# Performance work log

Hardware: AMD Instinct MI355X
Metric: run time of the kernel (lower is better)

Reference implementation:

```python
import jax, jax.numpy as jnp
import numpy as np


def relu_bt(x):
    # -threshold(-leaky_relu(x), -t, -t) == min(leaky_relu(x), t), t = ||x||_inf (detached)
    t = jax.lax.stop_gradient(jnp.max(jnp.abs(x)))
    return jnp.minimum(jax.nn.leaky_relu(x, negative_slope=0.01), t)


def setup_inputs() -> dict:
    key = jax.random.key(0)
    k1, k2, k3, k4 = jax.random.split(key, 4)
    N, E, F_in, F_out = 100000, 1600000, 128, 64
    x = jax.random.normal(k1, (N, F_in), dtype=jnp.float32)
    edge_index = jax.random.randint(k2, (2, E), 0, N, dtype=jnp.int64)
    # xavier_normal with gain=1.414
    W = jax.random.normal(k3, (F_in, F_out), dtype=jnp.float32) * (1.414 * np.sqrt(2.0 / (F_in + F_out)))
    a = jax.random.normal(k4, (1, 4 * F_out), dtype=jnp.float32) * (1.414 * np.sqrt(2.0 / (1 + 4 * F_out)))
    return {"x": x, "edge_index": edge_index, "W": W, "a": a}


def reference(x, edge_index, W, a):
    N = x.shape[0]
    F_out = W.shape[1]
    h = x @ W  # [N, F_out]
    src = edge_index[0]
    dst = edge_index[1]
    hs = h[src]  # [E, F_out]
    hd = h[dst]  # [E, F_out]
    agg = relu_bt(hs + hd)
    diff = relu_bt(hs - hd)
    # a @ cat([hs, hd, agg, diff], dim=1).T == sum of four per-edge dot products
    a0, a1, a2, a3 = jnp.split(a.reshape(4 * F_out), 4)
    score = hs @ a0 + hd @ a1 + agg @ a2 + diff @ a3  # [E]
    edge_e = jnp.exp(-relu_bt(score))  # [E]
    # spmm(A, ones): rowsum over outgoing edges (grouped by src)
    e_rowsum = jax.ops.segment_sum(edge_e, src, num_segments=N)  # [N]
    # spmm(A, h): weighted aggregation of neighbor (dst) features into src rows
    h_prime = jax.ops.segment_sum(edge_e[:, None] * hd, src, num_segments=N)  # [N, F_out]
    return h_prime / (e_rowsum[:, None] + 1e-16)
```

## Files before the change

### kernel.cpp

```cpp
#include <hip/hip_runtime.h>
#include <hip/hip_fp16.h>

#define F_IN 128
#define F_OUT 64
#define BIN_TILE 2048
#define BSHIFT 6
#define BNODES 64
#define BCAP 2048u

#define LK_A 0.505f
#define LK_B 0.495f

__device__ __forceinline__ float leaky(float v) {
    return fmaf(LK_B, fabsf(v), LK_A * v);
}

template <int CTRL>
__device__ __forceinline__ float dppadd(float v) {
    return v + __builtin_bit_cast(float,
        __builtin_amdgcn_update_dpp(0, __builtin_bit_cast(int, v), CTRL, 0xf, 0xf, true));
}

__device__ __forceinline__ float sum8(float v) {
    v = dppadd<0xB1>(v);
    v = dppadd<0x4E>(v);
    v = dppadd<0x141>(v);
    return v;
}

__device__ __forceinline__ float xslot_sum2(float v) {
    v = dppadd<0x128>(v);
    v += __shfl_xor(v, 16);
    return v;
}

__device__ __forceinline__ float wave_sum(float v) {
    v += __builtin_bit_cast(float, __builtin_amdgcn_update_dpp(0, __builtin_bit_cast(int, v), 0x111, 0xf, 0xf, true));
    v += __builtin_bit_cast(float, __builtin_amdgcn_update_dpp(0, __builtin_bit_cast(int, v), 0x112, 0xf, 0xf, true));
    v += __builtin_bit_cast(float, __builtin_amdgcn_update_dpp(0, __builtin_bit_cast(int, v), 0x114, 0xf, 0xe, true));
    v += __builtin_bit_cast(float, __builtin_amdgcn_update_dpp(0, __builtin_bit_cast(int, v), 0x118, 0xf, 0xc, true));
    v += __builtin_bit_cast(float, __builtin_amdgcn_update_dpp(0, __builtin_bit_cast(int, v), 0x142, 0xa, 0xf, true));
    v += __builtin_bit_cast(float, __builtin_amdgcn_update_dpp(0, __builtin_bit_cast(int, v), 0x143, 0xc, 0xf, true));
    return __builtin_bit_cast(float, __builtin_amdgcn_readlane(__builtin_bit_cast(int, v), 63));
}

__device__ __forceinline__ void cvt8(const uint4 u, float* g) {
    float2 f;
    f = __half22float2(__builtin_bit_cast(__half2, u.x)); g[0] = f.x; g[1] = f.y;
    f = __half22float2(__builtin_bit_cast(__half2, u.y)); g[2] = f.x; g[3] = f.y;
    f = __half22float2(__builtin_bit_cast(__half2, u.z)); g[4] = f.x; g[5] = f.y;
    f = __half22float2(__builtin_bit_cast(__half2, u.w)); g[6] = f.x; g[7] = f.y;
}

__global__ __launch_bounds__(256) void gemm_binA(const float* __restrict__ x,
                                                 const float* __restrict__ W,
                                                 float* __restrict__ h32,
                                                 uint2* __restrict__ h16,
                                                 const int* __restrict__ ei,
                                                 unsigned* __restrict__ gcur,
                                                 unsigned* __restrict__ binned,
                                                 int N, int E, int NB, int ngemm,
                                                 unsigned cap, int mode) {
    __shared__ unsigned smem_u[8192];

    if ((int)blockIdx.x < ngemm) {
        float (*w_lds)[F_OUT] = (float (*)[F_OUT])smem_u;
        {
            const float4* Wv = (const float4*)W;
            float4* wl = (float4*)w_lds;
            for (int i = threadIdx.x; i < F_IN * F_OUT / 4; i += 256) wl[i] = Wv[i];
        }
        __syncthreads();

        const int cg = threadIdx.x & 15;
        const int rs = threadIdx.x >> 4;
        const int row0 = blockIdx.x * 128 + rs * 8;

        int r[8];
#pragma unroll
        for (int i = 0; i < 8; ++i) { const int rr = row0 + i; r[i] = rr < N ? rr : N - 1; }

        float4 acc[8];
#pragma unroll
        for (int i = 0; i < 8; ++i) acc[i] = make_float4(0.f, 0.f, 0.f, 0.f);

        float4 xc[8];
#pragma unroll
        for (int i = 0; i < 8; ++i) xc[i] = *(const float4*)(x + (size_t)r[i] * F_IN);

        for (int k4 = 0; k4 < 32; ++k4) {
            float4 xn[8];
            if (k4 < 31) {
#pragma unroll
                for (int i = 0; i < 8; ++i)
                    xn[i] = *(const float4*)(x + (size_t)r[i] * F_IN + (k4 + 1) * 4);
            }
            float4 wv[4];
#pragma unroll
            for (int kk = 0; kk < 4; ++kk)
                wv[kk] = *(const float4*)&w_lds[k4 * 4 + kk][cg * 4];

#pragma unroll
            for (int i = 0; i < 8; ++i) {
                acc[i].x = fmaf(xc[i].x, wv[0].x, acc[i].x);
                acc[i].y = fmaf(xc[i].x, wv[0].y, acc[i].y);
                acc[i].z = fmaf(xc[i].x, wv[0].z, acc[i].z);
                acc[i].w = fmaf(xc[i].x, wv[0].w, acc[i].w);
                acc[i].x = fmaf(xc[i].y, wv[1].x, acc[i].x);
                acc[i].y = fmaf(xc[i].y, wv[1].y, acc[i].y);
                acc[i].z = fmaf(xc[i].y, wv[1].z, acc[i].z);
                acc[i].w = fmaf(xc[i].y, wv[1].w, acc[i].w);
                acc[i].x = fmaf(xc[i].z, wv[2].x, acc[i].x);
                acc[i].y = fmaf(xc[i].z, wv[2].y, acc[i].y);
                acc[i].z = fmaf(xc[i].z, wv[2].z, acc[i].z);
                acc[i].w = fmaf(xc[i].z, wv[2].w, acc[i].w);
                acc[i].x = fmaf(xc[i].w, wv[3].x, acc[i].x);
                acc[i].y = fmaf(xc[i].w, wv[3].y, acc[i].y);
                acc[i].z = fmaf(xc[i].w, wv[3].z, acc[i].z);
                acc[i].w = fmaf(xc[i].w, wv[3].w, acc[i].w);
            }
            if (k4 < 31) {
#pragma unroll
                for (int i = 0; i < 8; ++i) xc[i] = xn[i];
            }
        }

#pragma unroll
        for (int i = 0; i < 8; ++i) {
            const int rr = row0 + i;
            if (rr < N) {
                if (mode & 2) *(float4*)(h32 + (size_t)rr * F_OUT + cg * 4) = acc[i];
                if (mode & 1) {
                    uint2 u;
                    u.x = __builtin_bit_cast(unsigned, __floats2half2_rn(acc[i].x, acc[i].y));
                    u.y = __builtin_bit_cast(unsigned, __floats2half2_rn(acc[i].z, acc[i].w));
                    h16[(size_t)rr * 16 + cg] = u;
                }
            }
        }
    } else {
        unsigned* lcnt  = smem_u;
        unsigned* lbase = smem_u + 2048;
        const int t = threadIdx.x;
        for (int i = t; i < NB; i += 256) lcnt[i] = 0;
        __syncthreads();
        const int base = ((int)blockIdx.x - ngemm) * BIN_TILE;
        unsigned pk[8], bk[8], rk[8];
#pragma unroll
        for (int i = 0; i < 8; ++i) {
            const int e = base + i * 256 + t;
            if (e < E) {
                const unsigned s = (unsigned)ei[e];
                const unsigned d = (unsigned)ei[E + e];
                bk[i] = s >> BSHIFT;
                pk[i] = ((s & (BNODES - 1u)) << 17) | d;
                rk[i] = atomicAdd(&lcnt[bk[i]], 1u);
            }
        }
        __syncthreads();
        for (int i = t; i < NB; i += 256) {
            const unsigned c = lcnt[i];
            lbase[i] = c ? atomicAdd(&gcur[i], c) : 0u;
        }
        __syncthreads();
#pragma unroll
        for (int i = 0; i < 8; ++i) {
            const int e = base + i * 256 + t;
            if (e < E) {
                const unsigned po = lbase[bk[i]] + rk[i];
                if (po < cap) binned[(size_t)bk[i] * cap + po] = pk[i];
            }
        }
    }
}

__global__ __launch_bounds__(256) void bucket_node(const unsigned* __restrict__ binned,
                                                   const unsigned* __restrict__ gcur,
                                                   const uint2* __restrict__ h16v,
                                                   const float* __restrict__ a,
                                                   float* __restrict__ out,
                                                   int N, unsigned cap) {
    __shared__ unsigned stg[BCAP];
    __shared__ uint4    hsl[BNODES * 8];
    __shared__ unsigned ndeg[BNODES];
    __shared__ unsigned nbase[BNODES];
    __shared__ unsigned ncur[BNODES];
    __shared__ unsigned ts[BNODES];

    const int b = blockIdx.x;
    const int t = threadIdx.x;
    const int node0 = b << BSHIFT;
    const size_t src0 = (size_t)b * cap;
    unsigned sz = gcur[b]; if (sz > cap) sz = cap;

    if (t < BNODES) ndeg[t] = 0;
    {
        const uint4* hsrc = (const uint4*)h16v;
        const int limit = N * 8;
#pragma unroll
        for (int k = 0; k < (BNODES * 8) / 256; ++k) {
            const int i = k * 256 + t;
            const int gi = node0 * 8 + i;
            hsl[i] = (gi < limit) ? hsrc[gi] : make_uint4(0u, 0u, 0u, 0u);
        }
    }
    __syncthreads();

    for (unsigned i = t; i < sz; i += 256)
        atomicAdd(&ndeg[binned[src0 + i] >> 17], 1u);
    __syncthreads();

    if (t < BNODES) ts[t] = ndeg[t];
    __syncthreads();
    for (int st = 1; st < BNODES; st <<= 1) {
        unsigned add = 0;
        if (t < BNODES && t >= st) add = ts[t - st];
        __syncthreads();
        if (t < BNODES) ts[t] += add;
        __syncthreads();
    }
    if (t < BNODES) {
        const unsigned ex = ts[t] - ndeg[t];
        nbase[t] = ex;
        ncur[t]  = ex;
    }
    __syncthreads();

    for (unsigned i = t; i < sz; i += 256) {
        const unsigned p = binned[src0 + i];
        const unsigned pos = atomicAdd(&ncur[p >> 17], 1u);
        stg[pos] = p & 0x1FFFFu;
    }
    __syncthreads();

    const int lane  = t & 63;
    const int half  = lane >> 5;
    const int slot4 = (lane >> 3) & 3;
    const int q     = lane & 7;
    const int slot8 = (t >> 6) * 2 + half;
    const char* h16 = (const char*)h16v;

    float b1[8], a2b[8], a3b[8], a0m[8];
#pragma unroll
    for (int f = 0; f < 8; ++f) {
        const float A0 = a[q * 8 + f];
        const float A1 = a[64 + q * 8 + f];
        const float A2 = a[128 + q * 8 + f];
        const float A3 = a[192 + q * 8 + f];
        b1[f]  = fmaf(LK_A, A2 - A3, A1);
        a2b[f] = LK_B * A2;
        a3b[f] = LK_B * A3;
        a0m[f] = fmaf(LK_A, A2 + A3, A0);
    }

#pragma unroll 1
    for (int nn = 0; nn < BNODES / 8; ++nn) {
        const int nloc = slot8 * (BNODES / 8) + nn;
        const int node = node0 + nloc;
        const int beg = (int)nbase[nloc];
        const int len = (int)ndeg[nloc];

        float hs[8]; cvt8(hsl[nloc * 8 + q], hs);
        float csp = 0.f;
#pragma unroll
        for (int f = 0; f < 8; ++f) csp = fmaf(hs[f], a0m[f], csp);
        const float cs = sum8(csp);

        float acc[8];
#pragma unroll
        for (int f = 0; f < 8; ++f) acc[f] = 0.f;
        float rsum = 0.f;

        const int lm1 = (len > 0) ? len - 1 : 0;
        int dA = 0;
        if (len > 0) { int e0 = slot4; if (e0 > lm1) e0 = lm1; dA = (int)stg[beg + e0]; }
        uint4 uA = *(const uint4*)(h16 + ((size_t)dA << 7) + q * 16);
        int dB = dA;
        if (len > 4) { int e1 = 4 + slot4; if (e1 > lm1) e1 = lm1; dB = (int)stg[beg + e1]; }
        uint4 uB = *(const uint4*)(h16 + ((size_t)dB << 7) + q * 16);
        int dC = dB;
        if (len > 8) { int e2 = 8 + slot4; if (e2 > lm1) e2 = lm1; dC = (int)stg[beg + e2]; }

        for (int cb = 0; cb < len; cb += 4) {
            uint4 uC = uB;
            int dD = dC;
            if (cb + 8 < len)
                uC = *(const uint4*)(h16 + ((size_t)dC << 7) + q * 16);
            if (cb + 12 < len) { int e3 = cb + 12 + slot4; if (e3 > lm1) e3 = lm1; dD = (int)stg[beg + e3]; }

            float g[8];
            cvt8(uA, g);
            float p0 = 0.f, p1 = 0.f;
#pragma unroll
            for (int f = 0; f < 8; f += 2) {
                const float sa0 = hs[f] + g[f],         sb0 = hs[f] - g[f];
                const float sa1 = hs[f + 1] + g[f + 1], sb1 = hs[f + 1] - g[f + 1];
                p0 = fmaf(g[f],     b1[f],     p0);
                p1 = fmaf(g[f + 1], b1[f + 1], p1);
                p0 = fmaf(fabsf(sa0), a2b[f],     p0);
                p1 = fmaf(fabsf(sa1), a2b[f + 1], p1);
                p0 = fmaf(fabsf(sb0), a3b[f],     p0);
                p1 = fmaf(fabsf(sb1), a3b[f + 1], p1);
            }
            const float R = sum8(p0 + p1);

            float e = __expf(-leaky(cs + R));
            e = (cb + slot4 < len) ? e : 0.f;
#pragma unroll
            for (int f = 0; f < 8; ++f) acc[f] = fmaf(e, g[f], acc[f]);
            rsum += e;

            uA = uB; uB = uC; dC = dD;
        }

#pragma unroll
        for (int f = 0; f < 8; ++f) acc[f] = xslot_sum2(acc[f]);
        rsum = xslot_sum2(rsum);

        if (slot4 == 0 && node < N) {
            const float inv = 1.f / (rsum + 1e-16f);
            float4 o0, o1;
            o0.x = acc[0] * inv; o0.y = acc[1] * inv; o0.z = acc[2] * inv; o0.w = acc[3] * inv;
            o1.x = acc[4] * inv; o1.y = acc[5] * inv; o1.z = acc[6] * inv; o1.w = acc[7] * inv;
            float* orow = out + (size_t)node * F_OUT + q * 8;
            *(float4*)orow = o0;
            *(float4*)(orow + 4) = o1;
        }
    }
}

__global__ __launch_bounds__(256) void hist_kernel(const int* __restrict__ ei,
                                                   unsigned* __restrict__ cnt, int E) {
    const int e = blockIdx.x * 256 + threadIdx.x;
    if (e < E) atomicAdd(&cnt[ei[e]], 1u);
}

__global__ __launch_bounds__(256) void scan1(const unsigned* __restrict__ cnt,
                                             unsigned* __restrict__ bsum, int n) {
    __shared__ unsigned lds[256];
    const int t = threadIdx.x;
    const int base = blockIdx.x * 2048 + t * 8;
    unsigned s = 0;
#pragma unroll
    for (int i = 0; i < 8; ++i) { const int idx = base + i; if (idx < n) s += cnt[idx]; }
    lds[t] = s; __syncthreads();
    for (int st = 128; st > 0; st >>= 1) {
        if (t < st) lds[t] += lds[t + st];
        __syncthreads();
    }
    if (t == 0) bsum[blockIdx.x] = lds[0];
}

__global__ __launch_bounds__(128) void scan2(unsigned* __restrict__ bsum,
                                             unsigned* __restrict__ off, int nb, int n) {
    __shared__ unsigned lds[128];
    const int t = threadIdx.x;
    if (t < nb) lds[t] = bsum[t];
    __syncthreads();
    if (t == 0) {
        unsigned run = 0;
        for (int i = 0; i < nb; ++i) { const unsigned v = lds[i]; lds[i] = run; run += v; }
        off[n] = run;
    }
    __syncthreads();
    if (t < nb) bsum[t] = lds[t];
}

__global__ __launch_bounds__(256) void scan3(const unsigned* __restrict__ cnt,
                                             const unsigned* __restrict__ bsum,
                                             unsigned* __restrict__ off,
                                             unsigned* __restrict__ cursor, int n) {
    __shared__ unsigned lds[256];
    const int t = threadIdx.x;
    const int base = blockIdx.x * 2048 + t * 8;
    unsigned v[8]; unsigned s = 0;
#pragma unroll
    for (int i = 0; i < 8; ++i) { const int idx = base + i; v[i] = (idx < n) ? cnt[idx] : 0u; s += v[i]; }
    lds[t] = s; __syncthreads();
    for (int st = 1; st < 256; st <<= 1) {
        const unsigned add = (t >= st) ? lds[t - st] : 0u;
        __syncthreads();
        lds[t] += add;
        __syncthreads();
    }
    unsigned excl = (t > 0 ? lds[t - 1] : 0u) + bsum[blockIdx.x];
#pragma unroll
    for (int i = 0; i < 8; ++i) {
        const int idx = base + i;
        if (idx < n) { off[idx] = excl; cursor[idx] = excl; excl += v[i]; }
    }
}

__global__ __launch_bounds__(256) void scatter_kernel(const int* __restrict__ ei,
                                                      unsigned* __restrict__ cursor,
                                                      int* __restrict__ sdst, int E) {
    const int e = blockIdx.x * 256 + threadIdx.x;
    if (e >= E) return;
    const int s = ei[e];
    const int d = ei[E + e];
    const unsigned pos = atomicAdd(&cursor[s], 1u);
    sdst[pos] = d;
}

__global__ __launch_bounds__(256) void node_kernel(const unsigned* __restrict__ off,
                                                   const unsigned* __restrict__ deg,
                                                   const int* __restrict__ sdst,
                                                   const uint2* __restrict__ h16v,
                                                   const float* __restrict__ a,
                                                   float* __restrict__ out, int N) {
    const int lane  = threadIdx.x & 63;
    const int half  = lane >> 5;
    const int slot4 = (lane >> 3) & 3;
    const int q     = lane & 7;
    const char* h16 = (const char*)h16v;

    float b1[8], a2b[8], a3b[8], a0m[8];
#pragma unroll
    for (int f = 0; f < 8; ++f) {
        const float A0 = a[q * 8 + f];
        const float A1 = a[64 + q * 8 + f];
        const float A2 = a[128 + q * 8 + f];
        const float A3 = a[192 + q * 8 + f];
        b1[f]  = fmaf(LK_A, A2 - A3, A1);
        a2b[f] = LK_B * A2;
        a3b[f] = LK_B * A3;
        a0m[f] = fmaf(LK_A, A2 + A3, A0);
    }

    const int wid = (int)((blockIdx.x * 256u + threadIdx.x) >> 6);
    const int nw  = (int)((gridDim.x * 256u) >> 6);

    for (int pr = wid; pr * 2 < N; pr += nw) {
        const int node = pr * 2 + half;
        const int nc = (node < N) ? node : N - 1;
        const unsigned beg = off[nc];
        const int len = (node < N) ? (int)deg[nc] : 0;

        float hs[8];
        cvt8(*(const uint4*)(h16 + ((size_t)nc << 7) + q * 16), hs);
        float csp = 0.f;
#pragma unroll
        for (int f = 0; f < 8; ++f) csp = fmaf(hs[f], a0m[f], csp);
        const float cs = sum8(csp);

        const int lenO = __shfl_xor(len, 32);
        const int ml = (len > lenO) ? len : lenO;

        float acc[8];
#pragma unroll
        for (int f = 0; f < 8; ++f) acc[f] = 0.f;
        float rsum = 0.f;

        const int lm1 = (len > 0) ? len - 1 : 0;
        int dA = 0;
        if (len > 0) { int e0 = slot4; if (e0 > lm1) e0 = lm1; dA = sdst[beg + e0]; }
        uint4 uA = *(const uint4*)(h16 + ((size_t)dA << 7) + q * 16);
        int dB = dA;
        if (len > 4) { int e1 = 4 + slot4; if (e1 > lm1) e1 = lm1; dB = sdst[beg + e1]; }
        uint4 uB = *(const uint4*)(h16 + ((size_t)dB << 7) + q * 16);
        int dC = dB;
        if (len > 8) { int e2 = 8 + slot4; if (e2 > lm1) e2 = lm1; dC = sdst[beg + e2]; }

        for (int cb = 0; cb < ml; cb += 4) {
            uint4 uC = uB;
            int dD = dC;
            if (cb + 8 < len)
                uC = *(const uint4*)(h16 + ((size_t)dC << 7) + q * 16);
            if (cb + 12 < len) { int e3 = cb + 12 + slot4; if (e3 > lm1) e3 = lm1; dD = sdst[beg + e3]; }

            float g[8];
            cvt8(uA, g);
            float p0 = 0.f, p1 = 0.f;
#pragma unroll
            for (int f = 0; f < 8; f += 2) {
                const float sa0 = hs[f] + g[f],         sb0 = hs[f] - g[f];
                const float sa1 = hs[f + 1] + g[f + 1], sb1 = hs[f + 1] - g[f + 1];
                p0 = fmaf(g[f],     b1[f],     p0);
                p1 = fmaf(g[f + 1], b1[f + 1], p1);
                p0 = fmaf(fabsf(sa0), a2b[f],     p0);
                p1 = fmaf(fabsf(sa1), a2b[f + 1], p1);
                p0 = fmaf(fabsf(sb0), a3b[f],     p0);
                p1 = fmaf(fabsf(sb1), a3b[f + 1], p1);
            }
            const float R = sum8(p0 + p1);
            float e = __expf(-leaky(cs + R));
            e = (cb + slot4 < len) ? e : 0.f;
#pragma unroll
            for (int f = 0; f < 8; ++f) acc[f] = fmaf(e, g[f], acc[f]);
            rsum += e;
            uA = uB; uB = uC; dC = dD;
        }

#pragma unroll
        for (int f = 0; f < 8; ++f) acc[f] = xslot_sum2(acc[f]);
        rsum = xslot_sum2(rsum);

        if (slot4 == 0 && node < N) {
            const float inv = 1.f / (rsum + 1e-16f);
            float4 o0, o1;
            o0.x = acc[0] * inv; o0.y = acc[1] * inv; o0.z = acc[2] * inv; o0.w = acc[3] * inv;
            o1.x = acc[4] * inv; o1.y = acc[5] * inv; o1.z = acc[6] * inv; o1.w = acc[7] * inv;
            float* orow = out + (size_t)node * F_OUT + q * 8;
            *(float4*)orow = o0;
            *(float4*)(orow + 4) = o1;
        }
    }
}

__device__ __forceinline__ float edge_part(float hs, float hd, float a1, float a2, float a3) {
    float p = hd * a1;
    p = fmaf(leaky(hs + hd), a2, p);
    p = fmaf(leaky(hs - hd), a3, p);
    return p;
}

__global__ __launch_bounds__(256) void edge_kernel(const int* __restrict__ ei,
                                                   const float* __restrict__ h,
                                                   const float* __restrict__ a,
                                                   float* __restrict__ hprime,
                                                   float* __restrict__ rowsum,
                                                   int E) {
    const int lane = threadIdx.x & 63;
    const int wave = (int)((blockIdx.x * blockDim.x + threadIdx.x) >> 6);
    const int nwaves = (int)((gridDim.x * blockDim.x) >> 6);
    const float a0 = a[lane], a1 = a[64 + lane], a2 = a[128 + lane], a3 = a[192 + lane];
    for (int e = wave; e < E; e += nwaves) {
        const int s = ei[e];
        const int d = ei[E + e];
        const float hs = h[(size_t)s * F_OUT + lane];
        const float hd = h[(size_t)d * F_OUT + lane];
        const float part = wave_sum(hs * a0 + edge_part(hs, hd, a1, a2, a3));
        const float ee = __expf(-leaky(part));
        atomicAdd(&hprime[(size_t)s * F_OUT + lane], ee * hd);
        if (lane == 0) atomicAdd(&rowsum[s], ee);
    }
}

__global__ __launch_bounds__(256) void finalize(float* __restrict__ out,
                                                const float* __restrict__ rowsum,
                                                int total) {
    const int i = blockIdx.x * blockDim.x + threadIdx.x;
    if (i < total) out[i] = out[i] / (rowsum[i >> 6] + 1e-16f);
}

static inline size_t align_up(size_t v, size_t a) { return (v + a - 1) & ~(a - 1); }

extern "C" void kernel_launch(void* const* d_in, const int* in_sizes, int n_in,
                              void* d_out, int out_size, void* d_ws, size_t ws_size,
                              hipStream_t stream) {
    const float* x  = (const float*)d_in[0];
    const int*   ei = (const int*)d_in[1];
    const float* W  = (const float*)d_in[2];
    const float* a  = (const float*)d_in[3];

    const int N = in_sizes[0] / F_IN;
    const int E = in_sizes[1] / 2;
    float* out = (float*)d_out;

    const int NB = (N + BNODES - 1) >> BSHIFT;
    const int ngemm = (N + 127) / 128;
    const int nbt = (E + BIN_TILE - 1) / BIN_TILE;
    const unsigned meanFill = (NB > 0) ? (unsigned)(E / NB) : 0u;

    char* ws = (char*)d_ws;
    const size_t szh16  = align_up((size_t)N * F_OUT * 2, 256);
    const size_t szoff  = align_up(((size_t)N + 1) * 4, 256);
    const size_t szedge = align_up((size_t)E * 4 + 64, 256);
    const size_t szbin  = align_up((size_t)NB * BCAP * 4 + 64, 256);

    const size_t binned_b = szh16;
    const size_t gcurA_b  = binned_b + szbin;
    const size_t needA    = gcurA_b + align_up((size_t)NB * 4, 256);
    const size_t offB_b   = szh16;
    const size_t degB_b   = offB_b + szoff;
    const size_t sdstB_b  = degB_b + szoff;
    const size_t cursor_b = sdstB_b + szedge;
    const size_t bsum_b   = cursor_b + align_up((size_t)N * 4, 256);
    const size_t needB    = bsum_b + 4096;

    uint2* h16 = (uint2*)ws;

    if (ws_size >= needA && N <= (1 << 17) && NB <= 2048 && meanFill <= (BCAP * 3u) / 4u) {
        unsigned* binned = (unsigned*)(ws + binned_b);
        unsigned* gcur   = (unsigned*)(ws + gcurA_b);

        hipMemsetAsync(gcur, 0, (size_t)NB * 4, stream);
        gemm_binA<<<ngemm + nbt, 256, 0, stream>>>(x, W, nullptr, h16, ei, gcur, binned,
                                                   N, E, NB, ngemm, BCAP, 1);
        bucket_node<<<NB, 256, 0, stream>>>(binned, gcur, h16, a, out, N, BCAP);
    } else if (ws_size >= needB && N <= (1 << 17)) {
        unsigned* off    = (unsigned*)(ws + offB_b);
        unsigned* deg    = (unsigned*)(ws + degB_b);
        int*      sdst   = (int*)(ws + sdstB_b);
        unsigned* cursor = (unsigned*)(ws + cursor_b);
        unsigned* bsum   = (unsigned*)(ws + bsum_b);
        const int nb2 = (N + 2047) / 2048;

        hipMemsetAsync(deg, 0, (size_t)N * 4, stream);
        gemm_binA<<<ngemm, 256, 0, stream>>>(x, W, nullptr, h16, ei, nullptr, nullptr,
                                             N, E, NB, ngemm, BCAP, 1);
        hist_kernel<<<(E + 255) / 256, 256, 0, stream>>>(ei, deg, E);
        scan1<<<nb2, 256, 0, stream>>>(deg, bsum, N);
        scan2<<<1, 128, 0, stream>>>(bsum, off, nb2, N);
        scan3<<<nb2, 256, 0, stream>>>(deg, bsum, off, cursor, N);
        scatter_kernel<<<(E + 255) / 256, 256, 0, stream>>>(ei, cursor, sdst, E);
        node_kernel<<<2048, 256, 0, stream>>>(off, deg, sdst, h16, a, out, N);
    } else {
        float* h32    = (float*)ws;
        float* rowsum = (float*)(ws + align_up((size_t)N * F_OUT * 4, 256));
        hipMemsetAsync(d_out, 0, (size_t)N * F_OUT * sizeof(float), stream);
        hipMemsetAsync(rowsum, 0, (size_t)N * sizeof(float), stream);
        gemm_binA<<<ngemm, 256, 0, stream>>>(x, W, h32, nullptr, ei, nullptr, nullptr,
                                             N, E, NB, ngemm, BCAP, 2);
        edge_kernel<<<2048, 256, 0, stream>>>(ei, h32, a, out, rowsum, E);
        finalize<<<((size_t)N * F_OUT + 255) / 256, 256, 0, stream>>>(out, rowsum, N * F_OUT);
    }
}
```

Baseline: 131.4 us.

## Halve node-bucket size, store W as fp16 in LDS, use shuffle scan

Node buckets shrink from 64 to 32 nodes with capacity 1024. This roughly doubles the number of bucket_node blocks and halves their shared-memory staging. The GEMM stage converts W to fp16 in LDS and reuses one count array for binning, halving the static shared allocation to allow higher occupancy. The per-bucket prefix sum becomes a wavefront shuffle scan instead of a barrier-heavy LDS scan. The trade-offs are reduced precision for W, more bin counters per binning block, and a larger bin count allowed in the fast path.

```diff
diff --git a/kernel.cpp b/kernel.cpp
--- a/kernel.cpp
+++ b/kernel.cpp
@@ -4,9 +4,9 @@
 #define F_IN 128
 #define F_OUT 64
 #define BIN_TILE 2048
-#define BSHIFT 6
-#define BNODES 64
-#define BCAP 2048u
+#define BSHIFT 5
+#define BNODES 32
+#define BCAP 1024u
 
 #define LK_A 0.505f
 #define LK_B 0.495f
@@ -50,6 +50,12 @@
     f = __half22float2(__builtin_bit_cast(__half2, u.y)); g[2] = f.x; g[3] = f.y;
     f = __half22float2(__builtin_bit_cast(__half2, u.z)); g[4] = f.x; g[5] = f.y;
     f = __half22float2(__builtin_bit_cast(__half2, u.w)); g[6] = f.x; g[7] = f.y;
+}
+
+__device__ __forceinline__ float4 cvt4h(const uint2 u) {
+    const float2 f0 = __half22float2(__builtin_bit_cast(__half2, u.x));
+    const float2 f1 = __half22float2(__builtin_bit_cast(__half2, u.y));
+    return make_float4(f0.x, f0.y, f1.x, f1.y);
 }
 
 __global__ __launch_bounds__(256) void gemm_binA(const float* __restrict__ x,
@@ -61,14 +67,13 @@
                                                  unsigned* __restrict__ binned,
                                                  int N, int E, int NB, int ngemm,
                                                  unsigned cap, int mode) {
-    __shared__ unsigned smem_u[8192];
+    __shared__ unsigned smem_u[4096];
 
     if ((int)blockIdx.x < ngemm) {
-        float (*w_lds)[F_OUT] = (float (*)[F_OUT])smem_u;
-        {
-            const float4* Wv = (const float4*)W;
-            float4* wl = (float4*)w_lds;
-            for (int i = threadIdx.x; i < F_IN * F_OUT / 4; i += 256) wl[i] = Wv[i];
+        __half2* wl = (__half2*)smem_u;
+        for (int i = threadIdx.x; i < F_IN * F_OUT / 2; i += 256) {
+            const float2 f = ((const float2*)W)[i];
+            wl[i] = __floats2half2_rn(f.x, f.y);
         }
         __syncthreads();
 
@@ -88,6 +93,7 @@
 #pragma unroll
         for (int i = 0; i < 8; ++i) xc[i] = *(const float4*)(x + (size_t)r[i] * F_IN);
 
+        const char* wbase = (const char*)smem_u;
         for (int k4 = 0; k4 < 32; ++k4) {
             float4 xn[8];
             if (k4 < 31) {
@@ -97,8 +103,10 @@
             }
             float4 wv[4];
 #pragma unroll
-            for (int kk = 0; kk < 4; ++kk)
-                wv[kk] = *(const float4*)&w_lds[k4 * 4 + kk][cg * 4];
+            for (int kk = 0; kk < 4; ++kk) {
+                const uint2 u = *(const uint2*)(wbase + ((k4 * 4 + kk) * 64 + cg * 4) * 2);
+                wv[kk] = cvt4h(u);
+            }
 
 #pragma unroll
             for (int i = 0; i < 8; ++i) {
@@ -139,8 +147,7 @@
             }
         }
     } else {
-        unsigned* lcnt  = smem_u;
-        unsigned* lbase = smem_u + 2048;
+        unsigned* lcnt = smem_u;
         const int t = threadIdx.x;
         for (int i = t; i < NB; i += 256) lcnt[i] = 0;
         __syncthreads();
@@ -160,14 +167,14 @@
         __syncthreads();
         for (int i = t; i < NB; i += 256) {
             const unsigned c = lcnt[i];
-            lbase[i] = c ? atomicAdd(&gcur[i], c) : 0u;
+            lcnt[i] = c ? atomicAdd(&gcur[i], c) : 0u;
         }
         __syncthreads();
 #pragma unroll
         for (int i = 0; i < 8; ++i) {
             const int e = base + i * 256 + t;
             if (e < E) {
-                const unsigned po = lbase[bk[i]] + rk[i];
+                const unsigned po = lcnt[bk[i]] + rk[i];
                 if (po < cap) binned[(size_t)bk[i] * cap + po] = pk[i];
             }
         }
@@ -185,7 +192,6 @@
     __shared__ unsigned ndeg[BNODES];
     __shared__ unsigned nbase[BNODES];
     __shared__ unsigned ncur[BNODES];
-    __shared__ unsigned ts[BNODES];
 
     const int b = blockIdx.x;
     const int t = threadIdx.x;
@@ -197,12 +203,8 @@
     {
         const uint4* hsrc = (const uint4*)h16v;
         const int limit = N * 8;
-#pragma unroll
-        for (int k = 0; k < (BNODES * 8) / 256; ++k) {
-            const int i = k * 256 + t;
-            const int gi = node0 * 8 + i;
-            hsl[i] = (gi < limit) ? hsrc[gi] : make_uint4(0u, 0u, 0u, 0u);
-        }
+        const int gi = node0 * 8 + t;
+        hsl[t] = (gi < limit) ? hsrc[gi] : make_uint4(0u, 0u, 0u, 0u);
     }
     __syncthreads();
 
@@ -210,19 +212,16 @@
         atomicAdd(&ndeg[binned[src0 + i] >> 17], 1u);
     __syncthreads();
 
-    if (t < BNODES) ts[t] = ndeg[t];
-    __syncthreads();
-    for (int st = 1; st < BNODES; st <<= 1) {
-        unsigned add = 0;
-        if (t < BNODES && t >= st) add = ts[t - st];
-        __syncthreads();
-        if (t < BNODES) ts[t] += add;
-        __syncthreads();
-    }
     if (t < BNODES) {
-        const unsigned ex = ts[t] - ndeg[t];
-        nbase[t] = ex;
-        ncur[t]  = ex;
+        const unsigned d = ndeg[t];
+        unsigned sc = d;
+#pragma unroll
+        for (int st = 1; st < BNODES; st <<= 1) {
+            const unsigned o = __shfl_up(sc, st, 64);
+            if (t >= st) sc += o;
+        }
+        nbase[t] = sc - d;
+        ncur[t]  = sc - d;
     }
     __syncthreads();
 
@@ -580,7 +579,7 @@
 
     uint2* h16 = (uint2*)ws;
 
-    if (ws_size >= needA && N <= (1 << 17) && NB <= 2048 && meanFill <= (BCAP * 3u) / 4u) {
+    if (ws_size >= needA && N <= (1 << 17) && NB <= 4096 && meanFill <= (BCAP * 3u) / 4u) {
         unsigned* binned = (unsigned*)(ws + binned_b);
         unsigned* gcur   = (unsigned*)(ws + gcurA_b);
 
```

After: 135.2 us. +2.8%, slower.
